# Kernel optimization log

Hardware: AMD Instinct MI355X
Metric: run time of the kernel (lower is better)

Reference implementation:

```python
import jax, jax.numpy as jnp
import numpy as np

B, T, I, H = 128, 1024, 512, 512

def setup_inputs() -> dict:
    key = jax.random.key(0)
    ks = jax.random.split(key, 8)
    s_i = 1.0 / np.sqrt(I)
    s_h = 1.0 / np.sqrt(H)
    return {
        "x":  jax.random.normal(ks[0], (B, T, I), dtype=jnp.float32),
        "h0": jax.random.normal(ks[1], (B, H), dtype=jnp.float32),
        "c0": jax.random.normal(ks[2], (B, H), dtype=jnp.float32),
        "ctx": jax.random.normal(ks[3], (B, 50, H), dtype=jnp.float32),
        "Wi": jax.random.uniform(ks[4], (I, 4 * H), dtype=jnp.float32, minval=-s_i, maxval=s_i),
        "bi": jax.random.uniform(ks[5], (4 * H,), dtype=jnp.float32, minval=-s_i, maxval=s_i),
        "Wh": jax.random.uniform(ks[6], (H, 4 * H), dtype=jnp.float32, minval=-s_h, maxval=s_h),
        "bh": jax.random.uniform(ks[7], (4 * H,), dtype=jnp.float32, minval=-s_h, maxval=s_h),
    }

def reference(x, h0, c0, ctx, Wi, bi, Wh, bh):
    # ctx / ctx_mask are accepted but unused by the original forward.
    # Precompute input projections for all timesteps in one big GEMM: [B,T,4H]
    x_gates = jnp.einsum("bti,ig->btg", x, Wi) + bi + bh
    x_gates_t = jnp.swapaxes(x_gates, 0, 1)  # [T,B,4H]
    Hh = h0.shape[-1]

    def step(carry, xg):
        hx, cx = carry
        gates = xg + hx @ Wh  # [B,4H]
        i_g, f_g, c_g, o_g = jnp.split(gates, 4, axis=1)
        ingate = jax.nn.sigmoid(i_g)
        forgetgate = jax.nn.sigmoid(f_g)
        cellgate = jnp.tanh(c_g)
        outgate = jax.nn.sigmoid(o_g)
        cy = forgetgate * cx + ingate * cellgate
        hy = outgate * jnp.tanh(cy)
        return (hy, cy), hy

    (hy, cy), out_t = jax.lax.scan(step, (h0, c0), x_gates_t)
    output = jnp.swapaxes(out_t, 0, 1)  # batch_first: [B,T,H]
    return output, hy, cy
```

## Files before the change

### kernel.cpp

```cpp
#include <hip/hip_runtime.h>
#include <hip/hip_fp16.h>

typedef _Float16 f16x8 __attribute__((ext_vector_type(8)));
typedef float f32x4 __attribute__((ext_vector_type(4)));
typedef unsigned short u16x8 __attribute__((ext_vector_type(8)));
typedef unsigned short ushort_t;
typedef unsigned int uint32;

constexpr size_t BTH = 128ull * 1024ull * 512ull;

__device__ __forceinline__ ushort_t f2h(float f) {
  return __half_as_ushort(__float2half(f));
}

__global__ void cvt_xT(const float* __restrict__ x, ushort_t* __restrict__ xT) {
  int row = blockIdx.x * 4 + (threadIdx.x >> 6);
  int lane = threadIdx.x & 63;
  int b = row >> 10, t = row & 1023;
  const float* src = x + (size_t)row * 512 + lane * 8;
  float4 f0 = *(const float4*)src;
  float4 f1 = *(const float4*)(src + 4);
  u16x8 u;
  u[0] = f2h(f0.x); u[1] = f2h(f0.y); u[2] = f2h(f0.z); u[3] = f2h(f0.w);
  u[4] = f2h(f1.x); u[5] = f2h(f1.y); u[6] = f2h(f1.z); u[7] = f2h(f1.w);
  *(u16x8*)(xT + ((size_t)t * 128 + b) * 512 + lane * 8) = u;
}

template<bool XPRE>
__global__ __launch_bounds__(256, 1)
void lstm_rec(const float* __restrict__ x,
              const ushort_t* __restrict__ xT,
              const float* __restrict__ h0,
              const float* __restrict__ c0,
              const float* __restrict__ Wi,
              const float* __restrict__ bi,
              const float* __restrict__ Wh,
              const float* __restrict__ bh,
              float* __restrict__ out,
              uint32* __restrict__ hbuf32,
              uint32* __restrict__ flags)
{
  extern __shared__ char smem[];
  ushort_t* Wis = (ushort_t*)smem;
  ushort_t* Whs = (ushort_t*)(smem + 65536);
  ushort_t* hls = (ushort_t*)(smem + 131072);
  float*    gst = (float*)(smem + 147456);

  const int tid = threadIdx.x;
  const int lane = tid & 63;
  const int w = tid >> 6;
  const int l15 = lane & 15;
  const int hi = lane >> 4;
  const int bid = blockIdx.x;
  const int rg = bid & 7;
  const int cg = bid >> 3;
  const int rowbase = rg << 4;
  const int colbase = cg << 4;

  {
    const int j4 = (tid & 3) << 2;
    const int q  = (tid >> 2) & 3;
    const int kb = tid >> 4;
    const int gc = (q << 9) + colbase + j4;
    for (int i = 0; i < 32; ++i) {
      int k = kb + (i << 4);
      float4 wi4 = *(const float4*)(Wi + (size_t)k * 2048 + gc);
      float4 wh4 = *(const float4*)(Wh + (size_t)k * 2048 + gc);
      #pragma unroll
      for (int m = 0; m < 4; ++m) {
        int v = ((j4 + m) << 2) + q;
        int idx = (v << 9) + ((((k >> 3) ^ (v & 7)) << 3) | (k & 7));
        Wis[idx] = f2h(((const float*)&wi4)[m]);
        Whs[idx] = f2h(((const float*)&wh4)[m]);
      }
    }
  }

  const int myv = (w << 4) + l15;
  const int mygc = ((myv & 3) << 9) + colbase + (myv >> 2);
  const float biasv = bi[mygc] + bh[mygc];

  const int myrow = rowbase + l15;
  const int mycol = colbase + (w << 2) + hi;
  float c = c0[myrow * 512 + mycol];

  if (tid < 128) {
    int r = tid >> 3, c2 = tid & 7;
    int grow = rowbase + r;
    int gcol = colbase + (c2 << 1);
    uint32 lo  = f2h(h0[grow * 512 + gcol]);
    uint32 hi2 = f2h(h0[grow * 512 + gcol + 1]);
    __hip_atomic_store(hbuf32 + grow * 256 + (gcol >> 1), lo | (hi2 << 16),
                       __ATOMIC_RELAXED, __HIP_MEMORY_SCOPE_AGENT);
  }
  __syncthreads();
  uint32* const myflag = flags + (rg << 5) + cg;
  if (tid == 0)
    __hip_atomic_store(myflag, 1u, __ATOMIC_RELAXED, __HIP_MEMORY_SCOPE_AGENT);

  const size_t xT_lane = (size_t)(rowbase + l15) * 512 + (hi << 3);
  const float* xf_lane = x + ((size_t)(rowbase + l15) * 1024) * 512 + (hi << 3);
  uint32* const fl = flags + (rg << 5) + (lane & 31);
  const int rsw = l15 & 7;
  const int vsw = myv & 7;
  const ushort_t* wiB = Wis + (myv << 9);
  const ushort_t* whB = Whs + (myv << 9);
  const ushort_t* hrow = hls + (l15 << 9);

  for (int t = 0; t < 1024; ++t) {
    if (w == 0) {
      const uint32 tgt = (uint32)(t + 1);
      while (true) {
        uint32 f = __hip_atomic_load(fl, __ATOMIC_RELAXED, __HIP_MEMORY_SCOPE_AGENT);
        if (__all((int)(f >= tgt))) break;
      }
    }
    __syncthreads();

    {
      uint32* hsrc = hbuf32 + (t & 1) * 32768 + (rowbase << 8);
      #pragma unroll
      for (int i = 0; i < 16; ++i) {
        int flat = (i << 8) + tid;
        uint32 v = __hip_atomic_load(hsrc + flat, __ATOMIC_RELAXED, __HIP_MEMORY_SCOPE_AGENT);
        int r = flat >> 8, c32 = flat & 255;
        ((uint32*)hls)[(r << 8) + (((c32 >> 2) ^ (r & 7)) << 2) + (c32 & 3)] = v;
      }
    }
    __syncthreads();

    f32x4 aI0 = {0.f, 0.f, 0.f, 0.f}, aI1 = {0.f, 0.f, 0.f, 0.f};
    f32x4 aH0 = {biasv, biasv, biasv, biasv}, aH1 = {0.f, 0.f, 0.f, 0.f};
    const ushort_t* xrow = XPRE ? xT + (((size_t)t) << 16) + xT_lane : nullptr;
    const float* xrf = XPRE ? nullptr : xf_lane + (((size_t)t) << 9);
    #pragma unroll
    for (int kk = 0; kk < 16; ++kk) {
      const int k0 = kk << 5;
      f16x8 ah = *(const f16x8*)(hrow + ((((kk << 2) + hi) ^ rsw) << 3));
      f16x8 ax;
      if (XPRE) {
        ax = *(const f16x8*)(xrow + k0);
      } else {
        float4 xa = *(const float4*)(xrf + k0);
        float4 xb = *(const float4*)(xrf + k0 + 4);
        ax[0] = (_Float16)xa.x; ax[1] = (_Float16)xa.y;
        ax[2] = (_Float16)xa.z; ax[3] = (_Float16)xa.w;
        ax[4] = (_Float16)xb.x; ax[5] = (_Float16)xb.y;
        ax[6] = (_Float16)xb.z; ax[7] = (_Float16)xb.w;
      }
      const int bofs = (((kk << 2) + hi) ^ vsw) << 3;
      f16x8 bI = *(const f16x8*)(wiB + bofs);
      f16x8 bH = *(const f16x8*)(whB + bofs);
      if (kk & 1) {
        aI1 = __builtin_amdgcn_mfma_f32_16x16x32_f16(ax, bI, aI1, 0, 0, 0);
        aH1 = __builtin_amdgcn_mfma_f32_16x16x32_f16(ah, bH, aH1, 0, 0, 0);
      } else {
        aI0 = __builtin_amdgcn_mfma_f32_16x16x32_f16(ax, bI, aI0, 0, 0, 0);
        aH0 = __builtin_amdgcn_mfma_f32_16x16x32_f16(ah, bH, aH0, 0, 0, 0);
      }
    }
    f32x4 acc = (aI0 + aI1) + (aH0 + aH1);

    {
      float* gp = gst + w * 280 + l15 * 17 + (hi << 2);
      gp[0] = acc[0]; gp[1] = acc[1]; gp[2] = acc[2]; gp[3] = acc[3];
    }
    __syncthreads();
    const float* gq = gst + w * 280 + (hi << 2) * 17 + l15;
    const float gI = gq[0], gF = gq[17], gG = gq[34], gO = gq[51];

    const float ig = 1.f / (1.f + __expf(-gI));
    const float fg = 1.f / (1.f + __expf(-gF));
    const float gg = 1.f - 2.f / (1.f + __expf(2.f * gG));
    const float og = 1.f / (1.f + __expf(-gO));
    c = fg * c + ig * gg;
    const float hv = og * (1.f - 2.f / (1.f + __expf(2.f * c)));

    out[((size_t)myrow * 1024 + (size_t)t) * 512 + mycol] = hv;

    ushort_t hb = f2h(hv);
    uint32 pp = (uint32)__shfl_xor((int)(uint32)hb, 16);
    if ((hi & 1) == 0) {
      uint32 packed = ((pp & 0xffffu) << 16) | (uint32)hb;
      __hip_atomic_store(hbuf32 + ((t + 1) & 1) * 32768 + (myrow << 8) + (mycol >> 1),
                         packed, __ATOMIC_RELAXED, __HIP_MEMORY_SCOPE_AGENT);
    }
    if (t == 1023) {
      out[BTH + (size_t)myrow * 512 + mycol] = hv;
      out[BTH + 65536 + (size_t)myrow * 512 + mycol] = c;
    }
    __syncthreads();
    if (tid == 0)
      __hip_atomic_store(myflag, (uint32)(t + 2), __ATOMIC_RELAXED, __HIP_MEMORY_SCOPE_AGENT);
  }
}

extern "C" void kernel_launch(void* const* d_in, const int* in_sizes, int n_in,
                              void* d_out, int out_size, void* d_ws, size_t ws_size,
                              hipStream_t stream) {
  const float* x  = (const float*)d_in[0];
  const float* h0 = (const float*)d_in[1];
  const float* c0 = (const float*)d_in[2];
  const float* Wi = (const float*)d_in[4];
  const float* bi = (const float*)d_in[5];
  const float* Wh = (const float*)d_in[6];
  const float* bh = (const float*)d_in[7];
  float* out = (float*)d_out;

  char* ws = (char*)d_ws;
  uint32* flags = (uint32*)ws;
  uint32* hbuf32 = (uint32*)(ws + 4096);
  ushort_t* xT = (ushort_t*)(ws + (1u << 20));
  const size_t need_xpre = (1ull << 20) + 134217728ull;
  const bool xpre = ws_size >= need_xpre;

  hipMemsetAsync(ws, 0, 4096, stream);

  if (xpre) {
    cvt_xT<<<dim3(32768), dim3(256), 0, stream>>>(x, xT);
  }

  const int LDS_BYTES = 147456 + 4480;
  if (xpre) {
    hipFuncSetAttribute((const void*)lstm_rec<true>,
                        hipFuncAttributeMaxDynamicSharedMemorySize, LDS_BYTES);
    void* args[] = {(void*)&x, (void*)&xT, (void*)&h0, (void*)&c0, (void*)&Wi,
                    (void*)&bi, (void*)&Wh, (void*)&bh, (void*)&out,
                    (void*)&hbuf32, (void*)&flags};
    hipLaunchCooperativeKernel((const void*)lstm_rec<true>, dim3(256), dim3(256),
                               args, LDS_BYTES, stream);
  } else {
    hipFuncSetAttribute((const void*)lstm_rec<false>,
                        hipFuncAttributeMaxDynamicSharedMemorySize, LDS_BYTES);
    void* args[] = {(void*)&x, (void*)&xT, (void*)&h0, (void*)&c0, (void*)&Wi,
                    (void*)&bi, (void*)&Wh, (void*)&bh, (void*)&out,
                    (void*)&hbuf32, (void*)&flags};
    hipLaunchCooperativeKernel((const void*)lstm_rec<false>, dim3(256), dim3(256),
                               args, LDS_BYTES, stream);
  }
}
```

Baseline: 7.855 ms.

## Replace flag barrier with tagged h-words, XCC-local row groups, overlapped x-GEMM

```diff
diff --git a/kernel.cpp b/kernel.cpp
--- a/kernel.cpp
+++ b/kernel.cpp
@@ -6,11 +6,27 @@
 typedef unsigned short u16x8 __attribute__((ext_vector_type(8)));
 typedef unsigned short ushort_t;
 typedef unsigned int uint32;
+typedef uint32 u32x4 __attribute__((ext_vector_type(4)));
 
 constexpr size_t BTH = 128ull * 1024ull * 512ull;
 
 __device__ __forceinline__ ushort_t f2h(float f) {
   return __half_as_ushort(__float2half(f));
+}
+
+__device__ __forceinline__ u32x4 ld4t(const uint32* p, bool fast) {
+  u32x4 r;
+  if (fast) asm volatile("global_load_dwordx4 %0, %1, off sc0" : "=v"(r) : "v"(p));
+  else      asm volatile("global_load_dwordx4 %0, %1, off sc0 sc1" : "=v"(r) : "v"(p));
+  return r;
+}
+__device__ __forceinline__ void st1t(uint32* p, uint32 v, bool fast) {
+  if (fast) asm volatile("global_store_dword %0, %1, off sc0" :: "v"(p), "v"(v) : "memory");
+  else      asm volatile("global_store_dword %0, %1, off sc0 sc1" :: "v"(p), "v"(v) : "memory");
+}
+__device__ __forceinline__ void waitvm0() {
+  asm volatile("s_waitcnt vmcnt(0)" ::: "memory");
+  __builtin_amdgcn_sched_barrier(0);
 }
 
 __global__ void cvt_xT(const float* __restrict__ x, ushort_t* __restrict__ xT) {
@@ -37,25 +53,49 @@
               const float* __restrict__ Wh,
               const float* __restrict__ bh,
               float* __restrict__ out,
-              uint32* __restrict__ hbuf32,
-              uint32* __restrict__ flags)
+              uint32* __restrict__ hbuf,
+              uint32* __restrict__ ctrl)
 {
   extern __shared__ char smem[];
   ushort_t* Wis = (ushort_t*)smem;
   ushort_t* Whs = (ushort_t*)(smem + 65536);
   ushort_t* hls = (ushort_t*)(smem + 131072);
   float*    gst = (float*)(smem + 147456);
+  __shared__ int s_rg, s_cg, s_fast;
 
   const int tid = threadIdx.x;
   const int lane = tid & 63;
   const int w = tid >> 6;
   const int l15 = lane & 15;
   const int hi = lane >> 4;
-  const int bid = blockIdx.x;
-  const int rg = bid & 7;
-  const int cg = bid >> 3;
+
+  if (tid == 0) {
+    uint32 xcc;
+    asm volatile("s_getreg_b32 %0, hwreg(HW_REG_XCC_ID)" : "=s"(xcc));
+    xcc &= 7u;
+    uint32 rin = __hip_atomic_fetch_add(&ctrl[xcc], 1u, __ATOMIC_RELAXED, __HIP_MEMORY_SCOPE_AGENT);
+    uint32 ar  = __hip_atomic_fetch_add(&ctrl[8],   1u, __ATOMIC_RELAXED, __HIP_MEMORY_SCOPE_AGENT);
+    __hip_atomic_fetch_add(&ctrl[9], 1u, __ATOMIC_ACQ_REL, __HIP_MEMORY_SCOPE_AGENT);
+    while (__hip_atomic_load(&ctrl[9], __ATOMIC_ACQUIRE, __HIP_MEMORY_SCOPE_AGENT) < 256u)
+      __builtin_amdgcn_s_sleep(2);
+    bool bal = true;
+    for (int i = 0; i < 8; ++i)
+      bal &= (__hip_atomic_load(&ctrl[i], __ATOMIC_RELAXED, __HIP_MEMORY_SCOPE_AGENT) == 32u);
+    if (bal) { s_rg = (int)xcc;      s_cg = (int)rin;      s_fast = 1; }
+    else     { s_rg = (int)(ar >> 5); s_cg = (int)(ar & 31); s_fast = 0; }
+  }
+  __syncthreads();
+  const int rg = s_rg, cg = s_cg;
+  const bool fast = (s_fast != 0);
   const int rowbase = rg << 4;
   const int colbase = cg << 4;
+
+  const int myrow = rowbase + l15;
+  const int mycol = colbase + (w << 2) + hi;
+
+  uint32* wr0 = hbuf + ((size_t)rg << 13) + (l15 << 9) + mycol;
+  uint32* wr1 = hbuf + ((size_t)(8 + rg) << 13) + (l15 << 9) + mycol;
+  st1t(wr0, (1u << 16) | (uint32)f2h(h0[myrow * 512 + mycol]), fast);
 
   {
     const int j4 = (tid & 3) << 2;
@@ -68,8 +108,8 @@
       float4 wh4 = *(const float4*)(Wh + (size_t)k * 2048 + gc);
       #pragma unroll
       for (int m = 0; m < 4; ++m) {
-        int v = ((j4 + m) << 2) + q;
-        int idx = (v << 9) + ((((k >> 3) ^ (v & 7)) << 3) | (k & 7));
+        int v2 = ((j4 + m) << 2) + q;
+        int idx = (v2 << 9) + ((((k >> 3) ^ (v2 & 7)) << 3) | (k & 7));
         Wis[idx] = f2h(((const float*)&wi4)[m]);
         Whs[idx] = f2h(((const float*)&wh4)[m]);
       }
@@ -79,93 +119,97 @@
   const int myv = (w << 4) + l15;
   const int mygc = ((myv & 3) << 9) + colbase + (myv >> 2);
   const float biasv = bi[mygc] + bh[mygc];
-
-  const int myrow = rowbase + l15;
-  const int mycol = colbase + (w << 2) + hi;
   float c = c0[myrow * 512 + mycol];
-
-  if (tid < 128) {
-    int r = tid >> 3, c2 = tid & 7;
-    int grow = rowbase + r;
-    int gcol = colbase + (c2 << 1);
-    uint32 lo  = f2h(h0[grow * 512 + gcol]);
-    uint32 hi2 = f2h(h0[grow * 512 + gcol + 1]);
-    __hip_atomic_store(hbuf32 + grow * 256 + (gcol >> 1), lo | (hi2 << 16),
-                       __ATOMIC_RELAXED, __HIP_MEMORY_SCOPE_AGENT);
-  }
-  __syncthreads();
-  uint32* const myflag = flags + (rg << 5) + cg;
-  if (tid == 0)
-    __hip_atomic_store(myflag, 1u, __ATOMIC_RELAXED, __HIP_MEMORY_SCOPE_AGENT);
 
   const size_t xT_lane = (size_t)(rowbase + l15) * 512 + (hi << 3);
   const float* xf_lane = x + ((size_t)(rowbase + l15) * 1024) * 512 + (hi << 3);
-  uint32* const fl = flags + (rg << 5) + (lane & 31);
   const int rsw = l15 & 7;
   const int vsw = myv & 7;
   const ushort_t* wiB = Wis + (myv << 9);
   const ushort_t* whB = Whs + (myv << 9);
   const ushort_t* hrow = hls + (l15 << 9);
 
-  for (int t = 0; t < 1024; ++t) {
-    if (w == 0) {
-      const uint32 tgt = (uint32)(t + 1);
-      while (true) {
-        uint32 f = __hip_atomic_load(fl, __ATOMIC_RELAXED, __HIP_MEMORY_SCOPE_AGENT);
-        if (__all((int)(f >= tgt))) break;
-      }
-    }
-    __syncthreads();
-
-    {
-      uint32* hsrc = hbuf32 + (t & 1) * 32768 + (rowbase << 8);
-      #pragma unroll
-      for (int i = 0; i < 16; ++i) {
-        int flat = (i << 8) + tid;
-        uint32 v = __hip_atomic_load(hsrc + flat, __ATOMIC_RELAXED, __HIP_MEMORY_SCOPE_AGENT);
-        int r = flat >> 8, c32 = flat & 255;
-        ((uint32*)hls)[(r << 8) + (((c32 >> 2) ^ (r & 7)) << 2) + (c32 & 3)] = v;
-      }
-    }
-    __syncthreads();
-
-    f32x4 aI0 = {0.f, 0.f, 0.f, 0.f}, aI1 = {0.f, 0.f, 0.f, 0.f};
-    f32x4 aH0 = {biasv, biasv, biasv, biasv}, aH1 = {0.f, 0.f, 0.f, 0.f};
-    const ushort_t* xrow = XPRE ? xT + (((size_t)t) << 16) + xT_lane : nullptr;
-    const float* xrf = XPRE ? nullptr : xf_lane + (((size_t)t) << 9);
-    #pragma unroll
-    for (int kk = 0; kk < 16; ++kk) {
-      const int k0 = kk << 5;
-      f16x8 ah = *(const f16x8*)(hrow + ((((kk << 2) + hi) ^ rsw) << 3));
-      f16x8 ax;
-      if (XPRE) {
-        ax = *(const f16x8*)(xrow + k0);
-      } else {
+  __syncthreads();
+
+  auto x_gemm = [&](int t) -> f32x4 {
+    f32x4 a0 = {biasv, biasv, biasv, biasv}, a1 = {0.f, 0.f, 0.f, 0.f};
+    if (XPRE) {
+      const ushort_t* xrow = xT + (((size_t)t) << 16) + xT_lane;
+      #pragma unroll
+      for (int kk = 0; kk < 16; ++kk) {
+        f16x8 ax = *(const f16x8*)(xrow + (kk << 5));
+        f16x8 bI = *(const f16x8*)(wiB + ((((kk << 2) + hi) ^ vsw) << 3));
+        if (kk & 1) a1 = __builtin_amdgcn_mfma_f32_16x16x32_f16(ax, bI, a1, 0, 0, 0);
+        else        a0 = __builtin_amdgcn_mfma_f32_16x16x32_f16(ax, bI, a0, 0, 0, 0);
+      }
+    } else {
+      const float* xrf = xf_lane + (((size_t)t) << 9);
+      #pragma unroll
+      for (int kk = 0; kk < 16; ++kk) {
+        const int k0 = kk << 5;
         float4 xa = *(const float4*)(xrf + k0);
         float4 xb = *(const float4*)(xrf + k0 + 4);
+        f16x8 ax;
         ax[0] = (_Float16)xa.x; ax[1] = (_Float16)xa.y;
         ax[2] = (_Float16)xa.z; ax[3] = (_Float16)xa.w;
         ax[4] = (_Float16)xb.x; ax[5] = (_Float16)xb.y;
         ax[6] = (_Float16)xb.z; ax[7] = (_Float16)xb.w;
-      }
-      const int bofs = (((kk << 2) + hi) ^ vsw) << 3;
-      f16x8 bI = *(const f16x8*)(wiB + bofs);
-      f16x8 bH = *(const f16x8*)(whB + bofs);
-      if (kk & 1) {
-        aI1 = __builtin_amdgcn_mfma_f32_16x16x32_f16(ax, bI, aI1, 0, 0, 0);
-        aH1 = __builtin_amdgcn_mfma_f32_16x16x32_f16(ah, bH, aH1, 0, 0, 0);
-      } else {
-        aI0 = __builtin_amdgcn_mfma_f32_16x16x32_f16(ax, bI, aI0, 0, 0, 0);
-        aH0 = __builtin_amdgcn_mfma_f32_16x16x32_f16(ah, bH, aH0, 0, 0, 0);
-      }
-    }
-    f32x4 acc = (aI0 + aI1) + (aH0 + aH1);
+        f16x8 bI = *(const f16x8*)(wiB + ((((kk << 2) + hi) ^ vsw) << 3));
+        if (kk & 1) a1 = __builtin_amdgcn_mfma_f32_16x16x32_f16(ax, bI, a1, 0, 0, 0);
+        else        a0 = __builtin_amdgcn_mfma_f32_16x16x32_f16(ax, bI, a0, 0, 0, 0);
+      }
+    }
+    return a0 + a1;
+  };
+
+  f32x4 axb = x_gemm(0);
+
+  const uint32* rd0 = hbuf + ((size_t)rg << 13) + (tid << 2);
+  const uint32* rd1 = hbuf + ((size_t)(8 + rg) << 13) + (tid << 2);
+
+  for (int t = 0; t < 1024; ++t) {
+    {
+      const uint32* base = (t & 1) ? rd1 : rd0;
+      const uint32 etag = (uint32)(t + 1);
+      u32x4 v[8];
+      #pragma unroll
+      for (int j = 0; j < 8; ++j) v[j] = ld4t(base + (j << 10), fast);
+      waitvm0();
+      #pragma unroll
+      for (int j = 0; j < 8; ++j) {
+        u32x4 vv = v[j];
+        while (((vv[0] >> 16) != etag) | ((vv[1] >> 16) != etag) |
+               ((vv[2] >> 16) != etag) | ((vv[3] >> 16) != etag)) {
+          __builtin_amdgcn_s_sleep(1);
+          vv = ld4t(base + (j << 10), fast);
+          waitvm0();
+        }
+        const int w0 = (j << 10) + (tid << 2);
+        const int r = w0 >> 9;
+        const int c32 = (w0 & 511) >> 1;
+        uint32 p0 = (vv[0] & 0xffffu) | (vv[1] << 16);
+        uint32 p1 = (vv[2] & 0xffffu) | (vv[3] << 16);
+        uint32* dst = (uint32*)hls + (r << 8) + (((c32 >> 2) ^ (r & 7)) << 2) + (c32 & 3);
+        dst[0] = p0; dst[1] = p1;
+      }
+    }
+    __syncthreads();
+
+    f32x4 aH0 = axb, aH1 = {0.f, 0.f, 0.f, 0.f};
+    #pragma unroll
+    for (int kk = 0; kk < 16; ++kk) {
+      f16x8 ah = *(const f16x8*)(hrow + ((((kk << 2) + hi) ^ rsw) << 3));
+      f16x8 bH = *(const f16x8*)(whB + ((((kk << 2) + hi) ^ vsw) << 3));
+      if (kk & 1) aH1 = __builtin_amdgcn_mfma_f32_16x16x32_f16(ah, bH, aH1, 0, 0, 0);
+      else        aH0 = __builtin_amdgcn_mfma_f32_16x16x32_f16(ah, bH, aH0, 0, 0, 0);
+    }
+    f32x4 acc = aH0 + aH1;
+    __syncthreads();
 
     {
       float* gp = gst + w * 280 + l15 * 17 + (hi << 2);
       gp[0] = acc[0]; gp[1] = acc[1]; gp[2] = acc[2]; gp[3] = acc[3];
     }
-    __syncthreads();
     const float* gq = gst + w * 280 + (hi << 2) * 17 + l15;
     const float gI = gq[0], gF = gq[17], gG = gq[34], gO = gq[51];
 
@@ -176,22 +220,16 @@
     c = fg * c + ig * gg;
     const float hv = og * (1.f - 2.f / (1.f + __expf(2.f * c)));
 
-    out[((size_t)myrow * 1024 + (size_t)t) * 512 + mycol] = hv;
-
-    ushort_t hb = f2h(hv);
-    uint32 pp = (uint32)__shfl_xor((int)(uint32)hb, 16);
-    if ((hi & 1) == 0) {
-      uint32 packed = ((pp & 0xffffu) << 16) | (uint32)hb;
-      __hip_atomic_store(hbuf32 + ((t + 1) & 1) * 32768 + (myrow << 8) + (mycol >> 1),
-                         packed, __ATOMIC_RELAXED, __HIP_MEMORY_SCOPE_AGENT);
-    }
+    if (t < 1023) {
+      uint32 word = ((uint32)(t + 2) << 16) | (uint32)f2h(hv);
+      st1t((t & 1) ? wr0 : wr1, word, fast);
+    }
+    out[((size_t)myrow << 19) + ((size_t)t << 9) + mycol] = hv;
     if (t == 1023) {
       out[BTH + (size_t)myrow * 512 + mycol] = hv;
       out[BTH + 65536 + (size_t)myrow * 512 + mycol] = c;
     }
-    __syncthreads();
-    if (tid == 0)
-      __hip_atomic_store(myflag, (uint32)(t + 2), __ATOMIC_RELAXED, __HIP_MEMORY_SCOPE_AGENT);
+    if (t < 1023) axb = x_gemm(t + 1);
   }
 }
 
@@ -208,13 +246,13 @@
   float* out = (float*)d_out;
 
   char* ws = (char*)d_ws;
-  uint32* flags = (uint32*)ws;
-  uint32* hbuf32 = (uint32*)(ws + 4096);
+  uint32* ctrl = (uint32*)ws;
+  uint32* hbuf = (uint32*)(ws + 4096);
   ushort_t* xT = (ushort_t*)(ws + (1u << 20));
   const size_t need_xpre = (1ull << 20) + 134217728ull;
   const bool xpre = ws_size >= need_xpre;
 
-  hipMemsetAsync(ws, 0, 4096, stream);
+  hipMemsetAsync(ws, 0, 4096 + 524288, stream);
 
   if (xpre) {
     cvt_xT<<<dim3(32768), dim3(256), 0, stream>>>(x, xT);
@@ -226,7 +264,7 @@
                         hipFuncAttributeMaxDynamicSharedMemorySize, LDS_BYTES);
     void* args[] = {(void*)&x, (void*)&xT, (void*)&h0, (void*)&c0, (void*)&Wi,
                     (void*)&bi, (void*)&Wh, (void*)&bh, (void*)&out,
-                    (void*)&hbuf32, (void*)&flags};
+                    (void*)&hbuf, (void*)&ctrl};
     hipLaunchCooperativeKernel((const void*)lstm_rec<true>, dim3(256), dim3(256),
                                args, LDS_BYTES, stream);
   } else {
@@ -234,7 +272,7 @@
                         hipFuncAttributeMaxDynamicSharedMemorySize, LDS_BYTES);
     void* args[] = {(void*)&x, (void*)&xT, (void*)&h0, (void*)&c0, (void*)&Wi,
                     (void*)&bi, (void*)&Wh, (void*)&bh, (void*)&out,
-                    (void*)&hbuf32, (void*)&flags};
+                    (void*)&hbuf, (void*)&ctrl};
     hipLaunchCooperativeKernel((const void*)lstm_rec<false>, dim3(256), dim3(256),
                                args, LDS_BYTES, stream);
   }
```

New measurement: 7.320 ms. 6.8% less time.
